# Optimization experiments

Measured on AMD Instinct MI355X. Metric: run time of the kernel, lower is better.

Reference implementation:

```python
import jax, jax.numpy as jnp
import numpy as np

D_MODEL = 1024
N_HEADS = 16
D_HEAD = D_MODEL // N_HEADS


def setup_inputs() -> dict:
    key = jax.random.key(0)
    ks = jax.random.split(key, 11)
    B, T = 2, 2048
    s = 1.0 / np.sqrt(D_MODEL)
    return {
        "query": jax.random.normal(ks[0], (B, T, D_MODEL), dtype=jnp.float32),
        "key": jax.random.normal(ks[1], (B, T, D_MODEL), dtype=jnp.float32),
        "value": jax.random.normal(ks[2], (B, T, D_MODEL), dtype=jnp.float32),
        "Wq": jax.random.normal(ks[3], (D_MODEL, D_MODEL), dtype=jnp.float32) * s,
        "bq": jnp.zeros((D_MODEL,), dtype=jnp.float32),
        "Wk": jax.random.normal(ks[4], (D_MODEL, D_MODEL), dtype=jnp.float32) * s,
        "bk": jnp.zeros((D_MODEL,), dtype=jnp.float32),
        "Wv": jax.random.normal(ks[5], (D_MODEL, D_MODEL), dtype=jnp.float32) * s,
        "bv": jnp.zeros((D_MODEL,), dtype=jnp.float32),
        "Wh": jax.random.normal(ks[6], (D_MODEL, D_MODEL), dtype=jnp.float32) * s,
        "bh": jnp.zeros((D_MODEL,), dtype=jnp.float32),
    }


def reference(query, key, value, Wq, bq, Wk, bk, Wv, bv, Wh, bh):
    B, T_src, _ = query.shape
    T_dst = key.shape[1]
    # torch nn.Linear: y = x @ W.T + b
    Q = query @ Wq.T + bq          # (B, T_src, D)
    K = key @ Wk.T + bk            # (B, T_dst, D)
    V = value @ Wv.T + bv          # (B, T_dst, D)
    Q = Q.reshape(B, T_src, N_HEADS, D_HEAD).transpose(0, 2, 1, 3)  # (B,H,Ts,dh)
    K = K.reshape(B, T_dst, N_HEADS, D_HEAD).transpose(0, 2, 1, 3)  # (B,H,Td,dh)
    V = V.reshape(B, T_dst, N_HEADS, D_HEAD).transpose(0, 2, 1, 3)  # (B,H,Td,dh)
    dot = jnp.einsum("bhsd,bhtd->bhst", Q, K) / np.sqrt(D_HEAD)     # (B,H,Ts,Td)
    scores = jax.nn.softmax(dot, axis=-1)
    out = jnp.einsum("bhst,bhtd->bhsd", scores, V)  # (B,H,Ts,dh)
    # Faithful to source: reshape WITHOUT transposing heads back (source quirk)
    out = out.reshape(B, T_src, D_MODEL)
    return out @ Wh.T + bh
```

## Files before the change

kernel.cpp:

```cpp
#include <hip/hip_runtime.h>
#include <hip/hip_bf16.h>
#include <stdint.h>

typedef __attribute__((ext_vector_type(8))) short bf16x8;
typedef __attribute__((ext_vector_type(4))) short bf16x4;
typedef __attribute__((ext_vector_type(4))) float f32x4;
typedef __attribute__((ext_vector_type(16))) float f32x16;
typedef __attribute__((ext_vector_type(4))) unsigned int u32x4;
typedef __attribute__((ext_vector_type(2))) __bf16 bf16x2n;

#define DEVI __device__ __forceinline__

DEVI short f2b(float f) {
  union { float f; uint32_t u; } x; x.f = f;
  uint32_t r = x.u + 0x7fffu + ((x.u >> 16) & 1u);
  return (short)(r >> 16);
}

DEVI unsigned packbf(float a, float b) {
  bf16x2n v; v[0] = (__bf16)a; v[1] = (__bf16)b;
  return __builtin_bit_cast(unsigned, v);
}

DEVI float exp2f_(float x) {
#if __has_builtin(__builtin_amdgcn_exp2f)
  return __builtin_amdgcn_exp2f(x);
#else
  return __expf(x * 0.6931471805599453f);
#endif
}

DEVI void plswap(unsigned& a, unsigned& b) {
#if __has_builtin(__builtin_amdgcn_permlane32_swap)
  auto r = __builtin_amdgcn_permlane32_swap(a, b, false, false);
  a = r[0]; b = r[1];
#else
  asm volatile("s_nop 1\n\tv_permlane32_swap_b32 %0, %1\n\ts_nop 1" : "+v"(a), "+v"(b));
#endif
}

DEVI float xsum32(float x) {
  unsigned a = __builtin_bit_cast(unsigned, x), b = a;
  plswap(a, b);
  return __builtin_bit_cast(float, a) + __builtin_bit_cast(float, b);
}

DEVI void async16(const void* gsrc, void* lds) {
  __builtin_amdgcn_global_load_lds((__attribute__((address_space(1))) void*)gsrc,
                                   (__attribute__((address_space(3))) void*)lds,
                                   16, 0, 0);
}

__global__ __launch_bounds__(256) void cvt_all(const float* __restrict__ q,
                                               const float* __restrict__ k,
                                               const float* __restrict__ v,
                                               const float* __restrict__ wq,
                                               const float* __restrict__ wk,
                                               const float* __restrict__ wv,
                                               const float* __restrict__ wh,
                                               short* __restrict__ ws) {
  const size_t MT = 4096ull * 1024ull;
  int bid = blockIdx.x;
  const float* src; short* dst; int idx;
  if (bid < 6144) {
    int r = bid >> 11;
    src = (r == 0) ? q : (r == 1) ? k : v;
    dst = ws + (size_t)r * MT;
    idx = (bid & 2047) * 256 + threadIdx.x;
  } else {
    int r = (bid - 6144) >> 9;
    src = (r == 0) ? wq : (r == 1) ? wk : (r == 2) ? wv : wh;
    dst = ws + 3 * MT + (size_t)r * (1024 * 1024);
    idx = ((bid - 6144) & 511) * 256 + threadIdx.x;
  }
  f32x4 a = ((const f32x4*)src)[2 * idx];
  f32x4 b = ((const f32x4*)src)[2 * idx + 1];
  bf16x8 o;
  o[0]=f2b(a[0]); o[1]=f2b(a[1]); o[2]=f2b(a[2]); o[3]=f2b(a[3]);
  o[4]=f2b(b[0]); o[5]=f2b(b[1]); o[6]=f2b(b[2]); o[7]=f2b(b[3]);
  ((bf16x8*)dst)[idx] = o;
}

__global__ __launch_bounds__(256) void gemm_qkv(const short* __restrict__ A0,
                                                const short* __restrict__ A1,
                                                const short* __restrict__ A2,
                                                const short* __restrict__ W0,
                                                const short* __restrict__ W1,
                                                const short* __restrict__ W2,
                                                const float* __restrict__ b0,
                                                const float* __restrict__ b1,
                                                const float* __restrict__ b2,
                                                short* __restrict__ O0,
                                                short* __restrict__ O1,
                                                short* __restrict__ O2) {
  constexpr int Kd = 1024, Nd = 1024;
  const int z = blockIdx.z;
  const short* A  = (z == 0) ? A0 : (z == 1) ? A1 : A2;
  const short* Bt = (z == 0) ? W0 : (z == 1) ? W1 : W2;
  const float* bias = (z == 0) ? b0 : (z == 1) ? b1 : b2;

  __shared__ __attribute__((aligned(128))) char smem[32768];
  char* As = smem;
  char* Bs = smem + 16384;
  const int tid = threadIdx.x, lane = tid & 63, wave = tid >> 6;
  const int m0 = blockIdx.x * 128, n0 = blockIdx.y * 128;
  const int wr = wave >> 1, wc = wave & 1;

  f32x4 acc[4][4];
#pragma unroll
  for (int i = 0; i < 4; i++)
#pragma unroll
    for (int j = 0; j < 4; j++) acc[i][j] = (f32x4)0.0f;

  for (int k0 = 0; k0 < Kd; k0 += 64) {
#pragma unroll
    for (int it = 0; it < 4; ++it) {
      int ci = it * 256 + tid;
      int r = ci >> 3, c8 = ci & 7;
      int sc = c8 ^ (r & 7);
      async16((const char*)A + ((size_t)(m0 + r) * Kd + k0) * 2 + sc * 16,
              As + it * 4096 + wave * 1024);
      async16((const char*)Bt + ((size_t)(n0 + r) * Kd + k0) * 2 + sc * 16,
              Bs + it * 4096 + wave * 1024);
    }
    __syncthreads();
#pragma unroll
    for (int kk = 0; kk < 2; ++kk) {
      bf16x8 af[4], bf[4];
#pragma unroll
      for (int i = 0; i < 4; i++) {
        int r = wr * 64 + i * 16 + (lane & 15);
        int cb = (kk * 64 + ((lane >> 4) << 4)) ^ ((r & 7) << 4);
        af[i] = *(const bf16x8*)(As + r * 128 + cb);
      }
#pragma unroll
      for (int j = 0; j < 4; j++) {
        int r = wc * 64 + j * 16 + (lane & 15);
        int cb = (kk * 64 + ((lane >> 4) << 4)) ^ ((r & 7) << 4);
        bf[j] = *(const bf16x8*)(Bs + r * 128 + cb);
      }
#pragma unroll
      for (int i = 0; i < 4; i++)
#pragma unroll
        for (int j = 0; j < 4; j++)
          acc[i][j] = __builtin_amdgcn_mfma_f32_16x16x32_bf16(af[i], bf[j], acc[i][j], 0, 0, 0);
    }
    __syncthreads();
  }

  const float scale = (z == 0) ? 0.18033688011112043f : 1.0f;
#pragma unroll
  for (int i = 0; i < 4; i++) {
    int mbase = m0 + wr * 64 + i * 16 + ((lane >> 4) << 2);
#pragma unroll
    for (int j = 0; j < 4; j++) {
      int n = n0 + wc * 64 + j * 16 + (lane & 15);
      float bvf = bias[n];
      if (z < 2) {
        short* out = (z == 0) ? O0 : O1;
#pragma unroll
        for (int r = 0; r < 4; r++)
          out[(size_t)(mbase + r) * Nd + n] = f2b((acc[i][j][r] + bvf) * scale);
      } else {
        int b = mbase >> 11, t = mbase & 2047;
        bf16x4 pk;
#pragma unroll
        for (int r = 0; r < 4; r++) pk[r] = f2b(acc[i][j][r] + bvf);
        *(bf16x4*)(O2 + ((size_t)(b * 1024 + n)) * 2048 + t) = pk;
      }
    }
  }
}

__global__ __launch_bounds__(256) void gemm_out(const short* __restrict__ A,
                                                const short* __restrict__ Bt,
                                                const float* __restrict__ bias,
                                                float* __restrict__ out) {
  constexpr int Kd = 1024, Nd = 1024;
  __shared__ __attribute__((aligned(128))) char smem[32768];
  char* As = smem;
  char* Bs = smem + 16384;
  const int tid = threadIdx.x, lane = tid & 63, wave = tid >> 6;
  const int m0 = blockIdx.x * 128, n0 = blockIdx.y * 128;
  const int wr = wave >> 1, wc = wave & 1;

  f32x4 acc[4][4];
#pragma unroll
  for (int i = 0; i < 4; i++)
#pragma unroll
    for (int j = 0; j < 4; j++) acc[i][j] = (f32x4)0.0f;

  for (int k0 = 0; k0 < Kd; k0 += 64) {
#pragma unroll
    for (int it = 0; it < 4; ++it) {
      int ci = it * 256 + tid;
      int r = ci >> 3, c8 = ci & 7;
      int sc = c8 ^ (r & 7);
      async16((const char*)A + ((size_t)(m0 + r) * Kd + k0) * 2 + sc * 16,
              As + it * 4096 + wave * 1024);
      async16((const char*)Bt + ((size_t)(n0 + r) * Kd + k0) * 2 + sc * 16,
              Bs + it * 4096 + wave * 1024);
    }
    __syncthreads();
#pragma unroll
    for (int kk = 0; kk < 2; ++kk) {
      bf16x8 af[4], bf[4];
#pragma unroll
      for (int i = 0; i < 4; i++) {
        int r = wr * 64 + i * 16 + (lane & 15);
        int cb = (kk * 64 + ((lane >> 4) << 4)) ^ ((r & 7) << 4);
        af[i] = *(const bf16x8*)(As + r * 128 + cb);
      }
#pragma unroll
      for (int j = 0; j < 4; j++) {
        int r = wc * 64 + j * 16 + (lane & 15);
        int cb = (kk * 64 + ((lane >> 4) << 4)) ^ ((r & 7) << 4);
        bf[j] = *(const bf16x8*)(Bs + r * 128 + cb);
      }
#pragma unroll
      for (int i = 0; i < 4; i++)
#pragma unroll
        for (int j = 0; j < 4; j++)
          acc[i][j] = __builtin_amdgcn_mfma_f32_16x16x32_bf16(af[i], bf[j], acc[i][j], 0, 0, 0);
    }
    __syncthreads();
  }

#pragma unroll
  for (int i = 0; i < 4; i++) {
    int mbase = m0 + wr * 64 + i * 16 + ((lane >> 4) << 2);
#pragma unroll
    for (int j = 0; j < 4; j++) {
      int n = n0 + wc * 64 + j * 16 + (lane & 15);
      float bvf = bias[n];
#pragma unroll
      for (int r = 0; r < 4; r++)
        out[(size_t)(mbase + r) * Nd + n] = acc[i][j][r] + bvf;
    }
  }
}

__global__ __launch_bounds__(128) void attn_kernel(const short* __restrict__ Q,
                                                   const short* __restrict__ K,
                                                   const short* __restrict__ Vt,
                                                   short* __restrict__ X) {
  constexpr int T = 2048, D = 1024;
  __shared__ __attribute__((aligned(128))) char smem[32768];
  const int tid = threadIdx.x, lane = tid & 63, wave = tid >> 6;
  const int hi1 = lane >> 5, l31 = lane & 31;

  int bid0 = blockIdx.x;
  int bid = (bid0 & 7) * 128 + (bid0 >> 3);
  const int bh = bid >> 5, qt = bid & 31;
  const int b = bh >> 4, h = bh & 15;
  const int qrow = qt * 64 + wave * 32 + l31;

  bf16x8 qf[4];
  {
    const short* qptr = Q + ((size_t)(b * T + qrow)) * D + h * 64 + hi1 * 8;
#pragma unroll
    for (int kk = 0; kk < 4; kk++) qf[kk] = *(const bf16x8*)(qptr + kk * 16);
  }

  f32x16 o0 = (f32x16)0.0f, o1 = (f32x16)0.0f;
  f32x16 lvec = (f32x16)0.0f;

  const int swz = (l31 & 7) << 4;
  const int rK0 = l31 * 128, rK1 = (32 + l31) * 128;

  auto STAGE = [&](int bufi, int t0) {
    char* Kd = smem + bufi * 8192;
    char* Vd = smem + 16384 + bufi * 8192;
#pragma unroll
    for (int it = 0; it < 4; ++it) {
      int ci = it * 128 + tid;
      int r = ci >> 3, c8 = ci & 7;
      int sc = (c8 ^ (r & 7)) * 16;
      async16((const char*)(K + ((size_t)(b * T + t0 + r)) * D + h * 64) + sc,
              Kd + it * 2048 + wave * 1024);
      async16((const char*)(Vt + ((size_t)(b * 1024 + h * 64 + r)) * T + t0) + sc,
              Vd + it * 2048 + wave * 1024);
    }
  };

  STAGE(0, 0);

  for (int it = 0; it < 32; ++it) {
    const int cur = it & 1;
    __syncthreads();
    if (it < 31) STAGE(cur ^ 1, (it + 1) * 64);

    char* Kb = smem + cur * 8192;
    char* Vb = smem + 16384 + cur * 8192;

    f32x16 s0 = (f32x16)0.0f, s1 = (f32x16)0.0f;
    __builtin_amdgcn_s_setprio(1);
#pragma unroll
    for (int kk = 0; kk < 4; kk++) {
      int cb = (kk * 32 + hi1 * 16) ^ swz;
      bf16x8 ak0 = *(const bf16x8*)(Kb + rK0 + cb);
      s0 = __builtin_amdgcn_mfma_f32_32x32x16_bf16(ak0, qf[kk], s0, 0, 0, 0);
      bf16x8 ak1 = *(const bf16x8*)(Kb + rK1 + cb);
      s1 = __builtin_amdgcn_mfma_f32_32x32x16_bf16(ak1, qf[kk], s1, 0, 0, 0);
    }
    __builtin_amdgcn_s_setprio(0);

#pragma unroll
    for (int i = 0; i < 16; i++) {
      s0[i] = exp2f_(s0[i]);
      s1[i] = exp2f_(s1[i]);
    }
    lvec += s0;
    lvec += s1;

    unsigned w[16];
#pragma unroll
    for (int r2 = 0; r2 < 4; r2++)
#pragma unroll
      for (int wi = 0; wi < 2; wi++) {
        w[r2 * 2 + wi]     = packbf(s0[r2 * 4 + 2 * wi], s0[r2 * 4 + 2 * wi + 1]);
        w[8 + r2 * 2 + wi] = packbf(s1[r2 * 4 + 2 * wi], s1[r2 * 4 + 2 * wi + 1]);
      }
    bf16x8 ap[4];
#pragma unroll
    for (int kk = 0; kk < 4; kk++) {
      u32x4 t4;
#pragma unroll
      for (int wi = 0; wi < 2; wi++) {
        unsigned a = w[(kk >> 1) * 8 + (kk & 1) * 4 + wi];
        unsigned c = w[(kk >> 1) * 8 + (kk & 1) * 4 + 2 + wi];
        plswap(a, c);
        t4[wi] = a; t4[2 + wi] = c;
      }
      ap[kk] = __builtin_bit_cast(bf16x8, t4);
    }

    __builtin_amdgcn_s_setprio(1);
#pragma unroll
    for (int kk = 0; kk < 4; kk++) {
      int cb = (kk * 32 + hi1 * 16) ^ swz;
      bf16x8 av0 = *(const bf16x8*)(Vb + rK0 + cb);
      o0 = __builtin_amdgcn_mfma_f32_32x32x16_bf16(av0, ap[kk], o0, 0, 0, 0);
      bf16x8 av1 = *(const bf16x8*)(Vb + rK1 + cb);
      o1 = __builtin_amdgcn_mfma_f32_32x32x16_bf16(av1, ap[kk], o1, 0, 0, 0);
    }
    __builtin_amdgcn_s_setprio(0);
  }

  float l0 = (lvec[0] + lvec[1]) + (lvec[2] + lvec[3]);
  float l1 = (lvec[4] + lvec[5]) + (lvec[6] + lvec[7]);
  float l2 = (lvec[8] + lvec[9]) + (lvec[10] + lvec[11]);
  float l3 = (lvec[12] + lvec[13]) + (lvec[14] + lvec[15]);
  float l_run = xsum32((l0 + l1) + (l2 + l3));
  float inv = 1.0f / l_run;

  size_t xoff = ((size_t)(b * T + h * 128 + (qrow >> 4))) * D + ((qrow & 15) << 6) + hi1 * 4;
#pragma unroll
  for (int ntd = 0; ntd < 2; ntd++) {
#pragma unroll
    for (int rg = 0; rg < 4; rg++) {
      bf16x4 pk;
#pragma unroll
      for (int j = 0; j < 4; j++) {
        float v = (ntd == 0) ? o0[rg * 4 + j] : o1[rg * 4 + j];
        pk[j] = f2b(v * inv);
      }
      *(bf16x4*)(X + xoff + ntd * 32 + rg * 8) = pk;
    }
  }
}

extern "C" void kernel_launch(void* const* d_in, const int* in_sizes, int n_in,
                              void* d_out, int out_size, void* d_ws, size_t ws_size,
                              hipStream_t stream) {
  (void)in_sizes; (void)n_in; (void)out_size; (void)ws_size;
  const float* query = (const float*)d_in[0];
  const float* key   = (const float*)d_in[1];
  const float* value = (const float*)d_in[2];
  const float* Wq = (const float*)d_in[3];
  const float* bq = (const float*)d_in[4];
  const float* Wk = (const float*)d_in[5];
  const float* bk = (const float*)d_in[6];
  const float* Wv = (const float*)d_in[7];
  const float* bv = (const float*)d_in[8];
  const float* Wh = (const float*)d_in[9];
  const float* bh = (const float*)d_in[10];

  short* ws = (short*)d_ws;
  const size_t MT = 4096ull * 1024ull;
  short* qin_b = ws;
  short* kin_b = ws + MT;
  short* vin_b = ws + 2 * MT;
  short* Wq_b  = ws + 3 * MT;
  short* Wk_b  = Wq_b + 1024 * 1024;
  short* Wv_b  = Wk_b + 1024 * 1024;
  short* Wh_b  = Wv_b + 1024 * 1024;
  short* Qb    = ws + 4 * MT;
  short* Kb    = ws + 5 * MT;
  short* Vtb   = ws + 6 * MT;
  short* Xb    = ws + 7 * MT;

  cvt_all<<<8192, 256, 0, stream>>>(query, key, value, Wq, Wk, Wv, Wh, ws);

  gemm_qkv<<<dim3(32, 8, 3), 256, 0, stream>>>(qin_b, kin_b, vin_b,
                                               Wq_b, Wk_b, Wv_b,
                                               bq, bk, bv,
                                               Qb, Kb, Vtb);

  attn_kernel<<<1024, 128, 0, stream>>>(Qb, Kb, Vtb, Xb);

  gemm_out<<<dim3(32, 8), 256, 0, stream>>>(Xb, Wh_b, bh, (float*)d_out);
}
```

Baseline: 136.2 us.

## Split attention over key halves with 4-wave blocks and a combine kernel

```diff
diff --git a/kernel.cpp b/kernel.cpp
--- a/kernel.cpp
+++ b/kernel.cpp
@@ -15,6 +15,11 @@
   union { float f; uint32_t u; } x; x.f = f;
   uint32_t r = x.u + 0x7fffu + ((x.u >> 16) & 1u);
   return (short)(r >> 16);
+}
+
+DEVI float b2f(short s) {
+  union { uint32_t u; float f; } x; x.u = ((uint32_t)(uint16_t)s) << 16;
+  return x.f;
 }
 
 DEVI unsigned packbf(float a, float b) {
@@ -240,10 +245,13 @@
   }
 }
 
-__global__ __launch_bounds__(128) void attn_kernel(const short* __restrict__ Q,
-                                                   const short* __restrict__ K,
-                                                   const short* __restrict__ Vt,
-                                                   short* __restrict__ X) {
+__global__ __launch_bounds__(256) void attn_part(const short* __restrict__ Q,
+                                                 const short* __restrict__ K,
+                                                 const short* __restrict__ Vt,
+                                                 short* __restrict__ X0,
+                                                 short* __restrict__ X1,
+                                                 float* __restrict__ l0,
+                                                 float* __restrict__ l1) {
   constexpr int T = 2048, D = 1024;
   __shared__ __attribute__((aligned(128))) char smem[32768];
   const int tid = threadIdx.x, lane = tid & 63, wave = tid >> 6;
@@ -251,9 +259,15 @@
 
   int bid0 = blockIdx.x;
   int bid = (bid0 & 7) * 128 + (bid0 >> 3);
-  const int bh = bid >> 5, qt = bid & 31;
+  const int half = bid & 1;
+  const int qt = (bid >> 1) & 15;
+  const int bh = bid >> 5;
   const int b = bh >> 4, h = bh & 15;
-  const int qrow = qt * 64 + wave * 32 + l31;
+  const int qrow = qt * 128 + wave * 32 + l31;
+
+  short* Xh = half ? X1 : X0;
+  float* lh = half ? l1 : l0;
+  const int t00 = half * 1024;
 
   bf16x8 qf[4];
   {
@@ -268,27 +282,28 @@
   const int swz = (l31 & 7) << 4;
   const int rK0 = l31 * 128, rK1 = (32 + l31) * 128;
 
+  const char* Kbase = (const char*)(K + ((size_t)(b * T)) * D + h * 64);
+  const char* Vbase = (const char*)(Vt + ((size_t)(b * 1024 + h * 64)) * T);
+
   auto STAGE = [&](int bufi, int t0) {
     char* Kd = smem + bufi * 8192;
     char* Vd = smem + 16384 + bufi * 8192;
 #pragma unroll
-    for (int it = 0; it < 4; ++it) {
-      int ci = it * 128 + tid;
+    for (int it = 0; it < 2; ++it) {
+      int ci = it * 256 + tid;
       int r = ci >> 3, c8 = ci & 7;
-      int sc = (c8 ^ (r & 7)) * 16;
-      async16((const char*)(K + ((size_t)(b * T + t0 + r)) * D + h * 64) + sc,
-              Kd + it * 2048 + wave * 1024);
-      async16((const char*)(Vt + ((size_t)(b * 1024 + h * 64 + r)) * T + t0) + sc,
-              Vd + it * 2048 + wave * 1024);
+      int sc = (c8 ^ (r & 7)) << 4;
+      async16(Kbase + ((size_t)(t0 + r)) * 2048 + sc, Kd + it * 4096 + wave * 1024);
+      async16(Vbase + ((size_t)r) * 4096 + t0 * 2 + sc, Vd + it * 4096 + wave * 1024);
     }
   };
 
-  STAGE(0, 0);
-
-  for (int it = 0; it < 32; ++it) {
+  STAGE(0, t00);
+
+  for (int it = 0; it < 16; ++it) {
     const int cur = it & 1;
     __syncthreads();
-    if (it < 31) STAGE(cur ^ 1, (it + 1) * 64);
+    if (it < 15) STAGE(cur ^ 1, t00 + (it + 1) * 64);
 
     char* Kb = smem + cur * 8192;
     char* Vb = smem + 16384 + cur * 8192;
@@ -347,12 +362,12 @@
     __builtin_amdgcn_s_setprio(0);
   }
 
-  float l0 = (lvec[0] + lvec[1]) + (lvec[2] + lvec[3]);
-  float l1 = (lvec[4] + lvec[5]) + (lvec[6] + lvec[7]);
-  float l2 = (lvec[8] + lvec[9]) + (lvec[10] + lvec[11]);
-  float l3 = (lvec[12] + lvec[13]) + (lvec[14] + lvec[15]);
-  float l_run = xsum32((l0 + l1) + (l2 + l3));
-  float inv = 1.0f / l_run;
+  float la = (lvec[0] + lvec[1]) + (lvec[2] + lvec[3]);
+  float lb = (lvec[4] + lvec[5]) + (lvec[6] + lvec[7]);
+  float lc = (lvec[8] + lvec[9]) + (lvec[10] + lvec[11]);
+  float ld = (lvec[12] + lvec[13]) + (lvec[14] + lvec[15]);
+  float l_run = xsum32((la + lb) + (lc + ld));
+  lh[bh * 2048 + qrow] = l_run;
 
   size_t xoff = ((size_t)(b * T + h * 128 + (qrow >> 4))) * D + ((qrow & 15) << 6) + hi1 * 4;
 #pragma unroll
@@ -363,11 +378,32 @@
 #pragma unroll
       for (int j = 0; j < 4; j++) {
         float v = (ntd == 0) ? o0[rg * 4 + j] : o1[rg * 4 + j];
-        pk[j] = f2b(v * inv);
-      }
-      *(bf16x4*)(X + xoff + ntd * 32 + rg * 8) = pk;
-    }
-  }
+        pk[j] = f2b(v);
+      }
+      *(bf16x4*)(Xh + xoff + ntd * 32 + rg * 8) = pk;
+    }
+  }
+}
+
+__global__ __launch_bounds__(256) void attn_combine(const short* __restrict__ X0,
+                                                    const short* __restrict__ X1,
+                                                    const float* __restrict__ l0,
+                                                    const float* __restrict__ l1,
+                                                    short* __restrict__ X) {
+  int i8 = blockIdx.x * 256 + threadIdx.x;
+  int flat = i8 * 8;
+  int row = flat >> 10, col = flat & 1023;
+  int r2 = row & 2047;
+  int h = r2 >> 7, srow = r2 & 127;
+  int s = (srow << 4) | (col >> 6);
+  int bh = ((row >> 11) << 4) | h;
+  float inv = 1.0f / (l0[bh * 2048 + s] + l1[bh * 2048 + s]);
+  bf16x8 a = *(const bf16x8*)(X0 + flat);
+  bf16x8 c = *(const bf16x8*)(X1 + flat);
+  bf16x8 o;
+#pragma unroll
+  for (int j = 0; j < 8; j++) o[j] = f2b((b2f(a[j]) + b2f(c[j])) * inv);
+  *(bf16x8*)(X + flat) = o;
 }
 
 extern "C" void kernel_launch(void* const* d_in, const int* in_sizes, int n_in,
@@ -400,6 +436,11 @@
   short* Vtb   = ws + 6 * MT;
   short* Xb    = ws + 7 * MT;
 
+  short* X0 = qin_b;
+  short* X1 = kin_b;
+  float* l0 = (float*)vin_b;
+  float* l1 = l0 + 65536;
+
   cvt_all<<<8192, 256, 0, stream>>>(query, key, value, Wq, Wk, Wv, Wh, ws);
 
   gemm_qkv<<<dim3(32, 8, 3), 256, 0, stream>>>(qin_b, kin_b, vin_b,
@@ -407,7 +448,8 @@
                                                bq, bk, bv,
                                                Qb, Kb, Vtb);
 
-  attn_kernel<<<1024, 128, 0, stream>>>(Qb, Kb, Vtb, Xb);
+  attn_part<<<1024, 256, 0, stream>>>(Qb, Kb, Vtb, X0, X1, l0, l1);
+  attn_combine<<<2048, 256, 0, stream>>>(X0, X1, l0, l1, Xb);
 
   gemm_out<<<dim3(32, 8), 256, 0, stream>>>(Xb, Wh_b, bh, (float*)d_out);
 }
```

After: 137.2 us. About the same (+0.8%).
